# Kernel tuning notes

Measured on AMD Instinct MI355X. Metric: run time of the kernel, lower is better.

The kernel has to match this reference:

```python
import jax, jax.numpy as jnp
import numpy as np
import math

EMBED = 1024
HEADS = 16
HEAD_DIM = EMBED // HEADS  # 64
BSZ = 32
TGT = 512   # == src_len, required by the bmm-over-sequence structure
SRC = 512   # == BSZ*HEADS, required by the need_weights view


def _xavier(k, shape):
    fan_out, fan_in = shape
    limit = math.sqrt(6.0 / (fan_in + fan_out))
    return jax.random.uniform(k, shape, jnp.float32, -limit, limit)


def setup_inputs() -> dict:
    key = jax.random.key(0)
    ks = jax.random.split(key, 8)
    d = EMBED
    return {
        # query given as [bsz, tgt_len, d]; the module transposes it internally
        "query": jax.random.normal(ks[0], (BSZ, TGT, d), jnp.float32),
        "key": jax.random.normal(ks[1], (SRC, BSZ, d), jnp.float32),
        "value": jax.random.normal(ks[2], (SRC, BSZ, d), jnp.float32),
        "Wq": _xavier(ks[3], (d, d)), "bq": jnp.zeros((d,), jnp.float32),
        "Wk": _xavier(ks[4], (d, d)), "bk": jnp.zeros((d,), jnp.float32),
        "Wv": _xavier(ks[5], (d, d)), "bv": jnp.zeros((d,), jnp.float32),
        "Wo": _xavier(ks[6], (d, d)), "bo": jnp.zeros((d,), jnp.float32),
    }


def reference(query, key, value, Wq, bq, Wk, bk, Wv, bv, Wo, bo):
    H, hd = HEADS, HEAD_DIM
    # module transposes [bsz, tgt_len, d] -> [tgt_len, bsz, d]
    query = jnp.transpose(query, (1, 0, 2))
    T, B, D = query.shape
    S = key.shape[0]  # == T and == B*H by construction
    # projections (nn.Linear: x @ W.T + b)
    q = (query @ Wq.T + bq).reshape(T, B * H, hd)
    k = (key @ Wk.T + bk).reshape(S, B * H, hd)
    v = (value @ Wv.T + bv).reshape(S, B * H, hd)
    # torch.bmm with the SEQUENCE dim as the bmm batch dim (faithful to source):
    # scores: [T, BH, BH]
    scores = jnp.einsum('tbd,tcd->tbc', q, k) / jnp.sqrt(jnp.asarray(hd, q.dtype))
    attn = jax.nn.softmax(scores, axis=-1)  # dropout p=0.0, eval mode
    out = jnp.einsum('tbc,tcd->tbd', attn, v)  # [T, BH, hd]
    out = out.reshape(T, B, D) @ Wo.T + bo     # [T, B, D]
    # need_weights=True branch: view [T,H,B,S], permute(2,1,0,3), mean over heads
    w = attn.reshape(T, H, B, S).transpose(2, 1, 0, 3).mean(axis=1)  # [B, T, S]
    return out, w
```

## Files before the change

kernel.cpp:

```cpp
#include <hip/hip_runtime.h>
#include <hip/hip_bf16.h>
#include <stdint.h>


typedef __attribute__((ext_vector_type(8))) short bf16x8;
typedef __attribute__((ext_vector_type(4))) float f32x4;
typedef unsigned short u16;
typedef unsigned int u32;

typedef __attribute__((address_space(1))) const unsigned int as1_u32;
typedef __attribute__((address_space(3))) unsigned int as3_u32;

__device__ __forceinline__ void glds16(const void* g, void* l) {
    __builtin_amdgcn_global_load_lds((as1_u32*)g, (as3_u32*)l, 16, 0, 0);
}

__device__ __forceinline__ u16 f2bf(float f) {
    u32 u = __builtin_bit_cast(u32, f);
    u32 r = (u + 0x7FFFu + ((u >> 16) & 1u)) >> 16;
    return (u16)r;
}

template <int CTRL>
__device__ __forceinline__ float dpp_add(float x) {
    int xi = __builtin_bit_cast(int, x);
    int yi = __builtin_amdgcn_update_dpp(0, xi, CTRL, 0xF, 0xF, true);
    return x + __builtin_bit_cast(float, yi);
}
__device__ __forceinline__ float red16(float v) {
    v = dpp_add<0xB1>(v);
    v = dpp_add<0x4E>(v);
    v = dpp_add<0x141>(v);
    v = dpp_add<0x140>(v);
    return v;
}

__global__ void convw_kernel(const float4* __restrict__ query,
                             const float4* __restrict__ key,
                             const float4* __restrict__ value,
                             const float4* __restrict__ Wq, const float4* __restrict__ Wk,
                             const float4* __restrict__ Wv, const float4* __restrict__ Wo,
                             uint2* __restrict__ qx, uint2* __restrict__ kx,
                             uint2* __restrict__ vx,
                             uint2* __restrict__ wqb, uint2* __restrict__ wkb,
                             uint2* __restrict__ wvb, uint2* __restrict__ wob) {
    const int NT = gridDim.x * blockDim.x;
    for (int i = blockIdx.x * blockDim.x + threadIdx.x; i < 13631488; i += NT) {
        float4 v; uint2* d; int di;
        if (i < 4194304) {
            int m = i >> 8, c4 = i & 255;
            int t = m >> 5, b = m & 31;
            v = query[(b * 512 + t) * 256 + c4];
            d = qx; di = i;
        } else if (i < 8388608) {
            di = i - 4194304; v = key[di]; d = kx;
        } else if (i < 12582912) {
            di = i - 8388608; v = value[di]; d = vx;
        } else {
            int jj = i - 12582912;
            int wsel = jj >> 18; di = jj & 262143;
            const float4* s = wsel == 0 ? Wq : wsel == 1 ? Wk : wsel == 2 ? Wv : Wo;
            d = wsel == 0 ? wqb : wsel == 1 ? wkb : wsel == 2 ? wvb : wob;
            v = s[di];
        }
        uint2 r;
        r.x = (u32)f2bf(v.x) | ((u32)f2bf(v.y) << 16);
        r.y = (u32)f2bf(v.z) | ((u32)f2bf(v.w) << 16);
        d[di] = r;
    }
}

template <int F32OUT>
__global__ __launch_bounds__(256, 2)
void gemm_bb(const u16* __restrict__ A0, const u16* __restrict__ A1,
             const u16* __restrict__ A2,
             const u16* __restrict__ B0, const u16* __restrict__ B1,
             const u16* __restrict__ B2,
             const float* __restrict__ b0, const float* __restrict__ b1,
             const float* __restrict__ b2,
             void* __restrict__ C0, void* __restrict__ C1, void* __restrict__ C2) {
    __shared__ __align__(16) u16 As[2][8192];
    __shared__ __align__(16) u16 Bs[2][8192];
    const int z = blockIdx.z;
    const u16* A = z == 0 ? A0 : z == 1 ? A1 : A2;
    const u16* B = z == 0 ? B0 : z == 1 ? B1 : B2;
    const float* bias = z == 0 ? b0 : z == 1 ? b1 : b2;
    void* Cp = z == 0 ? C0 : z == 1 ? C1 : C2;
    const int tid = threadIdx.x;
    const int id = blockIdx.x;
    const int xcd = id & 7, j = id >> 3;
    const int ny = j & 7, band = xcd * 16 + (j >> 3);
    const long N0 = (long)ny * 128;
    const long M0 = (long)band * 128;
    const int lane = tid & 63, wv = tid >> 6;
    const int l15 = lane & 15, g = lane >> 4;
    const int wm = (wv >> 1) * 64, wn = (wv & 1) * 64;

    auto gldsAB = [&](int kt, int buf) {
#pragma unroll
        for (int i2 = 0; i2 < 4; ++i2) {
            int q = tid + 256 * i2; int r = q >> 3, c16 = q & 7;
            int c16s = c16 ^ (r & 7);
            char* lbA = (char*)As[buf] + (i2 * 256 + wv * 64) * 16;
            char* lbB = (char*)Bs[buf] + (i2 * 256 + wv * 64) * 16;
            glds16(A + (M0 + r) * 1024 + kt * 64 + c16s * 8, lbA);
            glds16(B + (N0 + r) * 1024 + kt * 64 + c16s * 8, lbB);
        }
    };
    gldsAB(0, 0);
    __syncthreads();
    f32x4 acc[4][4] = {};
    const int swz = (l15 & 7) << 4;
    for (int kt = 0; kt < 16; ++kt) {
        if (kt < 15) gldsAB(kt + 1, (kt + 1) & 1);
        const char* Acur = (const char*)As[kt & 1];
        const char* Bcur = (const char*)Bs[kt & 1];
#pragma unroll
        for (int kk = 0; kk < 2; ++kk) {
            bf16x8 av[4], bvv[4];
#pragma unroll
            for (int mt = 0; mt < 4; ++mt) {
                int row = wm + mt * 16 + l15;
                av[mt] = *(const bf16x8*)(Acur + row * 128 + ((kk * 64 + g * 16) ^ swz));
            }
#pragma unroll
            for (int nt = 0; nt < 4; ++nt) {
                int row = wn + nt * 16 + l15;
                bvv[nt] = *(const bf16x8*)(Bcur + row * 128 + ((kk * 64 + g * 16) ^ swz));
            }
#pragma unroll
            for (int mt = 0; mt < 4; ++mt)
#pragma unroll
                for (int nt = 0; nt < 4; ++nt)
                    acc[mt][nt] = __builtin_amdgcn_mfma_f32_16x16x32_bf16(av[mt], bvv[nt], acc[mt][nt], 0, 0, 0);
        }
        __syncthreads();
    }
    float bsv[4];
#pragma unroll
    for (int nt = 0; nt < 4; ++nt) bsv[nt] = bias[N0 + wn + nt * 16 + l15];
#pragma unroll
    for (int mt = 0; mt < 4; ++mt)
#pragma unroll
        for (int nt = 0; nt < 4; ++nt)
#pragma unroll
            for (int r = 0; r < 4; ++r) {
                long m = M0 + wm + mt * 16 + g * 4 + r;
                long n = N0 + wn + nt * 16 + l15;
                float v = acc[mt][nt][r] + bsv[nt];
                if (F32OUT) ((float*)Cp)[m * 1024 + n] = v;
                else        ((u16*)Cp)[m * 1024 + n] = f2bf(v);
            }
}

__global__ __launch_bounds__(256)
void vtrans_kernel(const u16* __restrict__ v_ws, u16* __restrict__ vt) {
    __shared__ __align__(16) u16 tl[64][136];
    const int bid = blockIdx.x;
    const int t = bid >> 2, c0 = (bid & 3) * 128;
    const u16* src = v_ws + (size_t)t * 32768 + (size_t)c0 * 64;
#pragma unroll
    for (int i = 0; i < 4; ++i) {
        int ch = i * 256 + threadIdx.x;
        int rc = ch >> 3, e0 = (ch & 7) * 8;
        bf16x8 v8 = *(const bf16x8*)(src + rc * 64 + e0);
#pragma unroll
        for (int j = 0; j < 8; ++j) tl[e0 + j][rc] = (u16)v8[j];
    }
    __syncthreads();
    u16* dst = vt + (size_t)t * 32768 + c0;
#pragma unroll
    for (int i = 0; i < 4; ++i) {
        int ch = i * 256 + threadIdx.x;
        int e = ch >> 4, cc = (ch & 15) * 8;
        *(bf16x8*)(dst + (size_t)e * 512 + cc) = *(const bf16x8*)(&tl[e][cc]);
    }
}

__global__ __launch_bounds__(512, 2)
void attn_kernel(const u16* __restrict__ Q, const u16* __restrict__ K,
                 const u16* __restrict__ VT, u16* __restrict__ ctx,
                 float* __restrict__ wout) {
    __shared__ __align__(16) char smem[32768];
    const int bid = blockIdx.x;
    const int wk_ = (bid & 7) * 256 + (bid >> 3);
    const int t = wk_ >> 2, it = wk_ & 3;
    const int tid = threadIdx.x, lane = tid & 63, wv = tid >> 6;
    const int l15 = lane & 15, g = lane >> 4;
    const int swk = (l15 & 7) << 4;
    const int bb = it * 8 + wv;
    const float ksc = 0.18033688011112042f;

    const u16* Kt = K + (size_t)t * 32768;
    const u16* Vtt = VT + (size_t)t * 32768;

    auto stageK = [&](int q, int slot) {
#pragma unroll
        for (int hh = 0; hh < 2; ++hh) {
            int idx = hh * 512 + tid;
            int sl = idx >> 3, c16 = idx & 7;
            int csw = c16 ^ (sl & 7);
            glds16(Kt + (size_t)(q * 128 + sl) * 64 + csw * 8,
                   smem + slot * 16384 + hh * 8192 + wv * 1024);
        }
    };
    auto stageV = [&](int q, int slot) {
#pragma unroll
        for (int hh = 0; hh < 2; ++hh) {
            int ch = hh * 512 + tid;
            int e = ch >> 4, c16 = ch & 15;
            glds16(Vtt + (size_t)e * 512 + q * 128 + ((c16 ^ (e & 7)) << 3),
                   smem + slot * 16384 + hh * 8192 + wv * 1024);
        }
    };
    f32x4 pv[4];
    auto pvQuarter = [&](const char* vb, bf16x8 p0, bf16x8 p1, bf16x8 p2, bf16x8 p3) {
        bf16x8 pq[4] = {p0, p1, p2, p3};
        __builtin_amdgcn_s_setprio(1);
#pragma unroll
        for (int m = 0; m < 4; ++m) {
#pragma unroll
            for (int nt = 0; nt < 4; ++nt) {
                int e = nt * 16 + l15;
                int esw = (e & 7) << 4;
                const char* vrow = vb + e * 256;
                union { bf16x8 v; uint2 uu[2]; } bv;
                bv.uu[0] = *(const uint2*)(vrow + ((m * 64 + 8 * g) ^ esw));
                bv.uu[1] = *(const uint2*)(vrow + ((m * 64 + 32 + 8 * g) ^ esw));
                pv[nt] = __builtin_amdgcn_mfma_f32_16x16x32_bf16(pq[m], bv.v, pv[nt], 0, 0, 0);
            }
        }
        __builtin_amdgcn_s_setprio(0);
    };

    const int c = 32 * l15 + bb;
    const u16* qrow = Q + ((size_t)t * 512 + c) * 64;
    bf16x8 qb0 = *(const bf16x8*)(qrow + g * 8);
    bf16x8 qb1 = *(const bf16x8*)(qrow + 32 + g * 8);

    stageK(0, 0);
    __syncthreads();
    float sum = 0.f;
    bf16x8 pP[16];
#pragma unroll
    for (int q = 0; q < 4; ++q) {
        if (q < 3) stageK(q + 1, (q + 1) & 1);
        else stageV(0, 0);
        const char* kb = smem + (q & 1) * 16384;
        __builtin_amdgcn_s_setprio(1);
#pragma unroll
        for (int m = 0; m < 4; ++m) {
            union { bf16x8 v; u32 u[4]; } pa;
#pragma unroll
            for (int h2 = 0; h2 < 2; ++h2) {
                int lsl = 2 * m + h2;
                const char* rowp = kb + (lsl * 16 + l15) * 128;
                bf16x8 a0 = *(const bf16x8*)(rowp + ((g * 16) ^ swk));
                bf16x8 a1 = *(const bf16x8*)(rowp + ((64 + g * 16) ^ swk));
                f32x4 zz = {0.f, 0.f, 0.f, 0.f};
                zz = __builtin_amdgcn_mfma_f32_16x16x32_bf16(a0, qb0, zz, 0, 0, 0);
                zz = __builtin_amdgcn_mfma_f32_16x16x32_bf16(a1, qb1, zz, 0, 0, 0);
                float e0 = exp2f(zz[0] * ksc), e1 = exp2f(zz[1] * ksc);
                float e2 = exp2f(zz[2] * ksc), e3 = exp2f(zz[3] * ksc);
                sum += (e0 + e1) + (e2 + e3);
                pa.u[2 * h2]     = (u32)f2bf(e0) | ((u32)f2bf(e1) << 16);
                pa.u[2 * h2 + 1] = (u32)f2bf(e2) | ((u32)f2bf(e3) << 16);
            }
            pP[q * 4 + m] = pa.v;
        }
        __builtin_amdgcn_s_setprio(0);
        __syncthreads();
    }
    sum += __shfl_xor(sum, 16);
    sum += __shfl_xor(sum, 32);
    const float inv = 1.f / sum;

    stageV(1, 1);

    {
        const float inv16 = inv * 0.0625f;
        float4 wreg0 = {0.f, 0.f, 0.f, 0.f}, wreg1 = {0.f, 0.f, 0.f, 0.f};
#pragma unroll
        for (int st = 0; st < 32; ++st) {
            union { bf16x8 v; u32 u[4]; } pu; pu.v = pP[st >> 1];
            u32 ua = pu.u[(st & 1) * 2], ub = pu.u[(st & 1) * 2 + 1];
            float v0 = __builtin_bit_cast(float, (ua & 0xFFFFu) << 16) * inv16;
            float v1 = __builtin_bit_cast(float, ua & 0xFFFF0000u) * inv16;
            float v2 = __builtin_bit_cast(float, (ub & 0xFFFFu) << 16) * inv16;
            float v3 = __builtin_bit_cast(float, ub & 0xFFFF0000u) * inv16;
            v0 = red16(v0); v1 = red16(v1); v2 = red16(v2); v3 = red16(v3);
            if ((st >> 1) == l15) {
                if (st & 1) wreg1 = (float4){v0, v1, v2, v3};
                else        wreg0 = (float4){v0, v1, v2, v3};
            }
        }
        float* wrow = wout + ((size_t)(bb * 512 + t)) * 512 + 32 * l15 + 4 * g;
        *(float4*)(wrow) = wreg0;
        *(float4*)(wrow + 16) = wreg1;
    }
    __syncthreads();

#pragma unroll
    for (int nt = 0; nt < 4; ++nt) pv[nt] = (f32x4){0.f, 0.f, 0.f, 0.f};
    pvQuarter(smem, pP[0], pP[1], pP[2], pP[3]);
    __syncthreads();
    stageV(2, 0);
    pvQuarter(smem + 16384, pP[4], pP[5], pP[6], pP[7]);
    __syncthreads();
    stageV(3, 1);
    pvQuarter(smem, pP[8], pP[9], pP[10], pP[11]);
    __syncthreads();
    pvQuarter(smem + 16384, pP[12], pP[13], pP[14], pP[15]);

    float invv[4];
#pragma unroll
    for (int r = 0; r < 4; ++r) invv[r] = __shfl(inv, g * 4 + r);
#pragma unroll
    for (int nt = 0; nt < 4; ++nt)
#pragma unroll
        for (int r = 0; r < 4; ++r)
            ctx[((size_t)t * 512 + 32 * (g * 4 + r) + bb) * 64 + nt * 16 + l15] =
                f2bf(pv[nt][r] * invv[r]);
}

extern "C" void kernel_launch(void* const* d_in, const int* in_sizes, int n_in,
                              void* d_out, int out_size, void* d_ws, size_t ws_size,
                              hipStream_t stream) {
    const float* query = (const float*)d_in[0];
    const float* key   = (const float*)d_in[1];
    const float* value = (const float*)d_in[2];
    const float* Wq = (const float*)d_in[3];  const float* bq = (const float*)d_in[4];
    const float* Wk = (const float*)d_in[5];  const float* bk = (const float*)d_in[6];
    const float* Wv = (const float*)d_in[7];  const float* bv = (const float*)d_in[8];
    const float* Wo = (const float*)d_in[9];  const float* bo = (const float*)d_in[10];

    char* ws = (char*)d_ws;
    u16* wqb  = (u16*)(ws + 0);
    u16* wkb  = (u16*)(ws + 2097152);
    u16* wvb  = (u16*)(ws + 4194304);
    u16* wob  = (u16*)(ws + 6291456);
    u16* q_ws = (u16*)(ws + 8388608);
    u16* k_ws = (u16*)(ws + 41943040);
    u16* v_ws = (u16*)(ws + 75497472);
    u16* qx   = (u16*)(ws + 109051904);

    float* out  = (float*)d_out;
    float* wout = out + 16777216;
    u16* kx = (u16*)d_out;
    u16* vx = (u16*)((char*)d_out + 33554432);
    u16* vt = (u16*)((char*)d_out + 33554432);

    convw_kernel<<<2048, 256, 0, stream>>>(
        (const float4*)query, (const float4*)key, (const float4*)value,
        (const float4*)Wq, (const float4*)Wk, (const float4*)Wv, (const float4*)Wo,
        (uint2*)qx, (uint2*)kx, (uint2*)vx,
        (uint2*)wqb, (uint2*)wkb, (uint2*)wvb, (uint2*)wob);

    dim3 gg3(1024, 1, 3);
    gemm_bb<0><<<gg3, 256, 0, stream>>>(qx, kx, vx, wqb, wkb, wvb,
                                        bq, bk, bv, q_ws, k_ws, v_ws);

    vtrans_kernel<<<2048, 256, 0, stream>>>(v_ws, vt);

    attn_kernel<<<2048, 512, 0, stream>>>(q_ws, k_ws, vt, q_ws, wout);

    gemm_bb<1><<<dim3(1024, 1, 1), 256, 0, stream>>>(q_ws, q_ws, q_ws,
                                                     wob, wob, wob, bo, bo, bo,
                                                     out, out, out);
}
```

Measured before the change: 372.4 us.

## Load whole K and V tiles into 64KB LDS instead of double-buffered quarters

Replaces the four-stage double-buffered K and V staging in the attention kernel with a single bulk load of the full 64KB K tile, then the full V tile, into a larger shared-memory buffer. This removes the per-quarter barriers and the staging lambdas, cutting synchronisation overhead. In exchange, the block now uses 64KB of LDS, which may limit resident blocks per CU (launch bounds ask for 2). The loads also no longer overlap with QK/PV compute, except that the V load is issued before the weight-output reduction.

```diff
diff --git a/kernel.cpp b/kernel.cpp
--- a/kernel.cpp
+++ b/kernel.cpp
@@ -181,7 +181,7 @@
 void attn_kernel(const u16* __restrict__ Q, const u16* __restrict__ K,
                  const u16* __restrict__ VT, u16* __restrict__ ctx,
                  float* __restrict__ wout) {
-    __shared__ __align__(16) char smem[32768];
+    __shared__ __align__(16) char smem[65536];
     const int bid = blockIdx.x;
     const int wk_ = (bid & 7) * 256 + (bid >> 3);
     const int t = wk_ >> 2, it = wk_ & 3;
@@ -194,89 +194,59 @@
     const u16* Kt = K + (size_t)t * 32768;
     const u16* Vtt = VT + (size_t)t * 32768;
 
-    auto stageK = [&](int q, int slot) {
-#pragma unroll
-        for (int hh = 0; hh < 2; ++hh) {
+    {
+#pragma unroll
+        for (int hh = 0; hh < 8; ++hh) {
             int idx = hh * 512 + tid;
             int sl = idx >> 3, c16 = idx & 7;
             int csw = c16 ^ (sl & 7);
-            glds16(Kt + (size_t)(q * 128 + sl) * 64 + csw * 8,
-                   smem + slot * 16384 + hh * 8192 + wv * 1024);
-        }
-    };
-    auto stageV = [&](int q, int slot) {
-#pragma unroll
-        for (int hh = 0; hh < 2; ++hh) {
-            int ch = hh * 512 + tid;
-            int e = ch >> 4, c16 = ch & 15;
-            glds16(Vtt + (size_t)e * 512 + q * 128 + ((c16 ^ (e & 7)) << 3),
-                   smem + slot * 16384 + hh * 8192 + wv * 1024);
-        }
-    };
-    f32x4 pv[4];
-    auto pvQuarter = [&](const char* vb, bf16x8 p0, bf16x8 p1, bf16x8 p2, bf16x8 p3) {
-        bf16x8 pq[4] = {p0, p1, p2, p3};
-        __builtin_amdgcn_s_setprio(1);
-#pragma unroll
-        for (int m = 0; m < 4; ++m) {
-#pragma unroll
-            for (int nt = 0; nt < 4; ++nt) {
-                int e = nt * 16 + l15;
-                int esw = (e & 7) << 4;
-                const char* vrow = vb + e * 256;
-                union { bf16x8 v; uint2 uu[2]; } bv;
-                bv.uu[0] = *(const uint2*)(vrow + ((m * 64 + 8 * g) ^ esw));
-                bv.uu[1] = *(const uint2*)(vrow + ((m * 64 + 32 + 8 * g) ^ esw));
-                pv[nt] = __builtin_amdgcn_mfma_f32_16x16x32_bf16(pq[m], bv.v, pv[nt], 0, 0, 0);
-            }
-        }
-        __builtin_amdgcn_s_setprio(0);
-    };
-
+            glds16(Kt + (size_t)sl * 64 + csw * 8, smem + hh * 8192 + wv * 1024);
+        }
+    }
     const int c = 32 * l15 + bb;
     const u16* qrow = Q + ((size_t)t * 512 + c) * 64;
     bf16x8 qb0 = *(const bf16x8*)(qrow + g * 8);
     bf16x8 qb1 = *(const bf16x8*)(qrow + 32 + g * 8);
-
-    stageK(0, 0);
-    __syncthreads();
+    __syncthreads();
+
     float sum = 0.f;
     bf16x8 pP[16];
-#pragma unroll
-    for (int q = 0; q < 4; ++q) {
-        if (q < 3) stageK(q + 1, (q + 1) & 1);
-        else stageV(0, 0);
-        const char* kb = smem + (q & 1) * 16384;
-        __builtin_amdgcn_s_setprio(1);
-#pragma unroll
-        for (int m = 0; m < 4; ++m) {
-            union { bf16x8 v; u32 u[4]; } pa;
-#pragma unroll
-            for (int h2 = 0; h2 < 2; ++h2) {
-                int lsl = 2 * m + h2;
-                const char* rowp = kb + (lsl * 16 + l15) * 128;
-                bf16x8 a0 = *(const bf16x8*)(rowp + ((g * 16) ^ swk));
-                bf16x8 a1 = *(const bf16x8*)(rowp + ((64 + g * 16) ^ swk));
-                f32x4 zz = {0.f, 0.f, 0.f, 0.f};
-                zz = __builtin_amdgcn_mfma_f32_16x16x32_bf16(a0, qb0, zz, 0, 0, 0);
-                zz = __builtin_amdgcn_mfma_f32_16x16x32_bf16(a1, qb1, zz, 0, 0, 0);
-                float e0 = exp2f(zz[0] * ksc), e1 = exp2f(zz[1] * ksc);
-                float e2 = exp2f(zz[2] * ksc), e3 = exp2f(zz[3] * ksc);
-                sum += (e0 + e1) + (e2 + e3);
-                pa.u[2 * h2]     = (u32)f2bf(e0) | ((u32)f2bf(e1) << 16);
-                pa.u[2 * h2 + 1] = (u32)f2bf(e2) | ((u32)f2bf(e3) << 16);
-            }
-            pP[q * 4 + m] = pa.v;
-        }
-        __builtin_amdgcn_s_setprio(0);
-        __syncthreads();
-    }
+    __builtin_amdgcn_s_setprio(1);
+#pragma unroll
+    for (int mq = 0; mq < 16; ++mq) {
+        union { bf16x8 v; u32 u[4]; } pa;
+#pragma unroll
+        for (int h2 = 0; h2 < 2; ++h2) {
+            int lsl = 2 * mq + h2;
+            const char* rowp = smem + (lsl * 16 + l15) * 128;
+            bf16x8 a0 = *(const bf16x8*)(rowp + ((g * 16) ^ swk));
+            bf16x8 a1 = *(const bf16x8*)(rowp + ((64 + g * 16) ^ swk));
+            f32x4 zz = {0.f, 0.f, 0.f, 0.f};
+            zz = __builtin_amdgcn_mfma_f32_16x16x32_bf16(a0, qb0, zz, 0, 0, 0);
+            zz = __builtin_amdgcn_mfma_f32_16x16x32_bf16(a1, qb1, zz, 0, 0, 0);
+            float e0 = exp2f(zz[0] * ksc), e1 = exp2f(zz[1] * ksc);
+            float e2 = exp2f(zz[2] * ksc), e3 = exp2f(zz[3] * ksc);
+            sum += (e0 + e1) + (e2 + e3);
+            pa.u[2 * h2]     = (u32)f2bf(e0) | ((u32)f2bf(e1) << 16);
+            pa.u[2 * h2 + 1] = (u32)f2bf(e2) | ((u32)f2bf(e3) << 16);
+        }
+        pP[mq] = pa.v;
+    }
+    __builtin_amdgcn_s_setprio(0);
     sum += __shfl_xor(sum, 16);
     sum += __shfl_xor(sum, 32);
     const float inv = 1.f / sum;
-
-    stageV(1, 1);
-
+    __syncthreads();
+
+    {
+#pragma unroll
+        for (int hh = 0; hh < 8; ++hh) {
+            int ch = hh * 512 + tid;
+            int e = ch >> 6, c6 = ch & 63;
+            int csw = c6 ^ (e & 7);
+            glds16(Vtt + (size_t)e * 512 + csw * 8, smem + hh * 8192 + wv * 1024);
+        }
+    }
     {
         const float inv16 = inv * 0.0625f;
         float4 wreg0 = {0.f, 0.f, 0.f, 0.f}, wreg1 = {0.f, 0.f, 0.f, 0.f};
@@ -300,17 +270,25 @@
     }
     __syncthreads();
 
+    f32x4 pv[4];
 #pragma unroll
     for (int nt = 0; nt < 4; ++nt) pv[nt] = (f32x4){0.f, 0.f, 0.f, 0.f};
-    pvQuarter(smem, pP[0], pP[1], pP[2], pP[3]);
-    __syncthreads();
-    stageV(2, 0);
-    pvQuarter(smem + 16384, pP[4], pP[5], pP[6], pP[7]);
-    __syncthreads();
-    stageV(3, 1);
-    pvQuarter(smem, pP[8], pP[9], pP[10], pP[11]);
-    __syncthreads();
-    pvQuarter(smem + 16384, pP[12], pP[13], pP[14], pP[15]);
+    __builtin_amdgcn_s_setprio(1);
+#pragma unroll
+    for (int mq = 0; mq < 16; ++mq) {
+        bf16x8 pa = pP[mq];
+#pragma unroll
+        for (int nt = 0; nt < 4; ++nt) {
+            int e = nt * 16 + l15;
+            const char* vrow = smem + e * 1024;
+            int off = mq * 64 + 8 * g;
+            union { bf16x8 v; uint2 uu[2]; } bv;
+            bv.uu[0] = *(const uint2*)(vrow + (off ^ swk));
+            bv.uu[1] = *(const uint2*)(vrow + ((off + 32) ^ swk));
+            pv[nt] = __builtin_amdgcn_mfma_f32_16x16x32_bf16(pa, bv.v, pv[nt], 0, 0, 0);
+        }
+    }
+    __builtin_amdgcn_s_setprio(0);
 
     float invv[4];
 #pragma unroll
```

Result: no change. 368.7 us (-1.0%).
